# Performance work log

Hardware: AMD Instinct MI355X
Metric: run time of the kernel (lower is better)

Reference implementation:

```python
import jax, jax.numpy as jnp
import numpy as np

B, L, S, H, E = 4, 2048, 2048, 8, 64


def setup_inputs() -> dict:
    key = jax.random.key(0)
    kq, kk, kv, kt = jax.random.split(key, 4)
    queries = jax.random.normal(kq, (B, L, H, E), dtype=jnp.float32)
    keys = jax.random.normal(kk, (B, S, H, E), dtype=jnp.float32)
    values = jax.random.normal(kv, (B, S, H, E), dtype=jnp.float32)
    # de-stationarization log-scale factor, kept small so exp(tau) ~ O(1)
    tau = 0.1 * jax.random.normal(kt, (B, 1, 1, 1), dtype=jnp.float32)
    # causal mask: True above the diagonal (positions to be masked)
    attn_mask = jnp.triu(jnp.ones((L, S), dtype=bool), k=1)
    return {"queries": queries, "keys": keys, "values": values,
            "attn_mask": attn_mask, "tau": tau}


def reference(queries, keys, values, attn_mask, tau):
    # queries: [B,L,H,E], keys/values: [B,S,H,E], tau: [B,1,1,1], mask: [L,S]
    E_ = queries.shape[-1]
    scale = 1.0 / jnp.sqrt(jnp.asarray(E_, dtype=queries.dtype))
    # scores: [B,H,L,S], with tau-based de-stationarization rescale
    scores = jnp.einsum('blhe,bshe->bhls', queries, keys) * (scale * jnp.exp(tau))
    scores = jnp.where(attn_mask, -jnp.inf, scores)
    A = jax.nn.softmax(scores, axis=-1)  # dropout is identity at inference
    V = jnp.einsum('bhls,bshd->blhd', A, values)
    return V
```

## Files before the change

### kernel.cpp

```cpp
#include <hip/hip_runtime.h>
#include <hip/hip_bf16.h>
#include <math.h>

#define B_ 4
#define L_ 2048
#define H_ 8
#define E_ 64
#define HE 512

typedef short bf16x8 __attribute__((ext_vector_type(8)));
typedef float f32x4 __attribute__((ext_vector_type(4)));
typedef float f32x2 __attribute__((ext_vector_type(2)));
typedef unsigned short u16x4 __attribute__((ext_vector_type(4)));
typedef unsigned short u16x8 __attribute__((ext_vector_type(8)));

__device__ __forceinline__ unsigned short f2b(float f) {
  return __builtin_bit_cast(unsigned short, (__hip_bfloat16)f);
}

__global__ __launch_bounds__(512, 4) void attn_fwd(
    const float* __restrict__ Q, const float* __restrict__ K,
    const float* __restrict__ V, const float* __restrict__ tau,
    float* __restrict__ O)
{
  const int f  = blockIdx.x + 16 * (blockIdx.y + 8 * blockIdx.z);
  const int u  = f >> 5, hb = f & 31;
  const int h  = hb & 7, b = hb >> 3;
  const int qt = (u < 8) ? u : 23 - u;

  const int tid  = threadIdx.x;
  const int wave = tid >> 6, lane = tid & 63;
  const int lg = lane >> 4, ll = lane & 15;
  const int llm = ll & 7;

  __shared__ unsigned short ldsK[2][64 * 64];
  __shared__ unsigned short ldsV[2][64 * 64];

  const float qscale = 0.125f * expf(tau[b]) * 1.44269504088896f;
  const int q0w = qt * 128 + wave * 16;

  const float* Qb = Q + (((size_t)b * L_ + (q0w + ll)) * H_ + h) * E_;
  bf16x8 qf[2];
  #pragma unroll
  for (int ek = 0; ek < 2; ++ek) {
    f32x4 a = *(const f32x4*)(Qb + ek * 32 + lg * 8);
    f32x4 c = *(const f32x4*)(Qb + ek * 32 + lg * 8 + 4);
    #pragma unroll
    for (int j = 0; j < 4; ++j) {
      qf[ek][j]     = (short)f2b(a[j] * qscale);
      qf[ek][4 + j] = (short)f2b(c[j] * qscale);
    }
  }

  float m_run = -INFINITY, l_run = 0.0f;
  f32x4 oacc[4];
  #pragma unroll
  for (int n = 0; n < 4; ++n) {
    oacc[n][0] = 0.f; oacc[n][1] = 0.f; oacc[n][2] = 0.f; oacc[n][3] = 0.f;
  }

  const int krow = tid >> 3;
  const int vq = tid >> 5,  vc = (tid & 31) * 2;
  const float* Kp = K + ((size_t)b * L_ * H_ + h) * E_ + (size_t)krow * HE + (tid & 7) * 8;
  const float* Vp = V + ((size_t)b * L_ * H_ + h) * E_ + (size_t)(4 * vq) * HE + vc;
  const int kw_off = krow * 64 + (((tid & 7) ^ (krow & 7)) << 3);

  const int nt = 2 * qt + 2;
  const int tmaxw = 2 * qt + (wave >> 2);

  {
    f32x4 k0 = *(const f32x4*)(Kp);
    f32x4 k1 = *(const f32x4*)(Kp + 4);
    f32x2 v0 = *(const f32x2*)(Vp);
    f32x2 v1 = *(const f32x2*)(Vp + HE);
    f32x2 v2 = *(const f32x2*)(Vp + 2 * HE);
    f32x2 v3 = *(const f32x2*)(Vp + 3 * HE);
    u16x8 kw;
    #pragma unroll
    for (int j = 0; j < 4; ++j) { kw[j] = f2b(k0[j]); kw[4 + j] = f2b(k1[j]); }
    *(u16x8*)(&ldsK[0][kw_off]) = kw;
    #pragma unroll
    for (int jj = 0; jj < 2; ++jj) {
      const int row = vc + jj;
      u16x4 vw;
      vw[0] = f2b(v0[jj]); vw[1] = f2b(v1[jj]);
      vw[2] = f2b(v2[jj]); vw[3] = f2b(v3[jj]);
      *(u16x4*)(&ldsV[0][row * 64 + (((vq >> 1) ^ (row & 7)) << 3) + 4 * (vq & 1)]) = vw;
    }
  }
  __syncthreads();
  int cur = 0;

  for (int t = 0; t < nt; ++t) {
    const bool havenext = (t + 1 < nt);
    f32x4 k0, k1; f32x2 v0, v1, v2, v3;
    if (havenext) {
      const float* Kn = Kp + (size_t)(t + 1) * 64 * HE;
      const float* Vn = Vp + (size_t)(t + 1) * 64 * HE;
      k0 = *(const f32x4*)(Kn);
      k1 = *(const f32x4*)(Kn + 4);
      v0 = *(const f32x2*)(Vn);
      v1 = *(const f32x2*)(Vn + HE);
      v2 = *(const f32x2*)(Vn + 2 * HE);
      v3 = *(const f32x2*)(Vn + 3 * HE);
    }

    if (t <= tmaxw) {
      const unsigned short* Kl = ldsK[cur];
      const unsigned short* Vl = ldsV[cur];

      f32x4 sacc[4];
      #pragma unroll
      for (int m = 0; m < 4; ++m) {
        sacc[m][0] = 0.f; sacc[m][1] = 0.f; sacc[m][2] = 0.f; sacc[m][3] = 0.f;
      }
      __builtin_amdgcn_s_setprio(1);
      #pragma unroll
      for (int ek = 0; ek < 2; ++ek) {
        #pragma unroll
        for (int m = 0; m < 4; ++m) {
          bf16x8 kf = *(const bf16x8*)(Kl + (16 * m + ll) * 64 +
                                       ((((ek << 2) + lg) ^ llm) << 3));
          sacc[m] = __builtin_amdgcn_mfma_f32_16x16x32_bf16(kf, qf[ek], sacc[m], 0, 0, 0);
        }
      }
      __builtin_amdgcn_s_setprio(0);

      if (t == tmaxw) {
        const int dq = q0w + ll - 64 * t;
        #pragma unroll
        for (int m = 0; m < 4; ++m)
          #pragma unroll
          for (int r = 0; r < 4; ++r)
            if (16 * m + 4 * lg + r > dq) sacc[m][r] = -3.0e38f;
      }

      float t0 = fmaxf(fmaxf(sacc[0][0], sacc[0][1]), fmaxf(sacc[0][2], sacc[0][3]));
      float t1 = fmaxf(fmaxf(sacc[1][0], sacc[1][1]), fmaxf(sacc[1][2], sacc[1][3]));
      float t2 = fmaxf(fmaxf(sacc[2][0], sacc[2][1]), fmaxf(sacc[2][2], sacc[2][3]));
      float t3 = fmaxf(fmaxf(sacc[3][0], sacc[3][1]), fmaxf(sacc[3][2], sacc[3][3]));
      float mx = fmaxf(fmaxf(t0, t1), fmaxf(t2, t3));
      mx = fmaxf(mx, __shfl_xor(mx, 16));
      mx = fmaxf(mx, __shfl_xor(mx, 32));

      if (!__all(mx - m_run <= 8.0f)) {
        const float mnew = fmaxf(m_run, mx);
        const float corr = exp2f(m_run - mnew);
        m_run = mnew;
        l_run *= corr;
        #pragma unroll
        for (int r = 0; r < 4; ++r) {
          const float cr = __shfl(corr, 4 * lg + r);
          #pragma unroll
          for (int n = 0; n < 4; ++n) oacc[n][r] *= cr;
        }
      }

      #pragma unroll
      for (int m = 0; m < 4; ++m)
        #pragma unroll
        for (int r = 0; r < 4; ++r)
          sacc[m][r] = exp2f(sacc[m][r] - m_run);

      float s0 = (sacc[0][0] + sacc[0][1]) + (sacc[0][2] + sacc[0][3]);
      float s1 = (sacc[1][0] + sacc[1][1]) + (sacc[1][2] + sacc[1][3]);
      float s2 = (sacc[2][0] + sacc[2][1]) + (sacc[2][2] + sacc[2][3]);
      float s3 = (sacc[3][0] + sacc[3][1]) + (sacc[3][2] + sacc[3][3]);
      float rs = (s0 + s1) + (s2 + s3);
      rs += __shfl_xor(rs, 16);
      rs += __shfl_xor(rs, 32);
      l_run += rs;

      bf16x8 pf[2];
      #pragma unroll
      for (int ek = 0; ek < 2; ++ek)
        #pragma unroll
        for (int r = 0; r < 4; ++r) {
          pf[ek][r]     = (short)f2b(sacc[2 * ek][r]);
          pf[ek][4 + r] = (short)f2b(sacc[2 * ek + 1][r]);
        }

      __builtin_amdgcn_s_setprio(1);
      #pragma unroll
      for (int ek = 0; ek < 2; ++ek) {
        #pragma unroll
        for (int n = 0; n < 4; ++n) {
          const int d = 16 * n + ll;
          const int base = d * 64 + 4 * (lg & 1);
          union { bf16x8 v8; u16x4 q[2]; } vu;
          vu.q[0] = *(const u16x4*)(Vl + base +
                       ((((ek << 2) + (lg >> 1)) ^ llm) << 3));
          vu.q[1] = *(const u16x4*)(Vl + base +
                       ((((ek << 2) + 2 + (lg >> 1)) ^ llm) << 3));
          oacc[n] = __builtin_amdgcn_mfma_f32_16x16x32_bf16(pf[ek], vu.v8, oacc[n], 0, 0, 0);
        }
      }
      __builtin_amdgcn_s_setprio(0);
    }

    if (havenext) {
      const int nb = cur ^ 1;
      u16x8 kw;
      #pragma unroll
      for (int j = 0; j < 4; ++j) { kw[j] = f2b(k0[j]); kw[4 + j] = f2b(k1[j]); }
      *(u16x8*)(&ldsK[nb][kw_off]) = kw;
      #pragma unroll
      for (int jj = 0; jj < 2; ++jj) {
        const int row = vc + jj;
        u16x4 vw;
        vw[0] = f2b(v0[jj]); vw[1] = f2b(v1[jj]);
        vw[2] = f2b(v2[jj]); vw[3] = f2b(v3[jj]);
        *(u16x4*)(&ldsV[nb][row * 64 + (((vq >> 1) ^ (row & 7)) << 3) + 4 * (vq & 1)]) = vw;
      }
      __syncthreads();
      cur = nb;
    }
  }

  const float linv = 1.0f / l_run;
  float* Ob = O + (((size_t)b * L_ + q0w) * H_ + h) * E_;
  #pragma unroll
  for (int r = 0; r < 4; ++r) {
    const float inv = __shfl(linv, 4 * lg + r);
    const int qrow = 4 * lg + r;
    #pragma unroll
    for (int n = 0; n < 4; ++n)
      Ob[(size_t)qrow * HE + 16 * n + ll] = oacc[n][r] * inv;
  }
}

extern "C" void kernel_launch(void* const* d_in, const int* in_sizes, int n_in,
                              void* d_out, int out_size, void* d_ws, size_t ws_size,
                              hipStream_t stream) {
  (void)in_sizes; (void)n_in; (void)out_size; (void)d_ws; (void)ws_size;
  const float* Q   = (const float*)d_in[0];
  const float* K   = (const float*)d_in[1];
  const float* V   = (const float*)d_in[2];
  const float* tau = (const float*)d_in[4];
  float* O = (float*)d_out;
  dim3 grid(L_ / 128, H_, B_), block(512);
  hipLaunchKernelGGL(attn_fwd, grid, block, 0, stream, Q, K, V, tau, O);
}
```

Measured before the change: 60.26 us.

## Switch attention to 32x32x16 MFMA with 4 waves of 32 query rows

Replaces the 16x16x32 bf16 MFMA tiling with 32x32x16 MFMA, so each wave handles 32 query rows and the block shrinks from 8 to 4 waves. P is converted to bf16 with packed v_cvt_pk_bf16_f32 and rearranged through v_permlane32_swap so it can feed the PV MFMA from registers. K/V staging loads are widened to full float4 per thread. Larger MFMA tiles cut LDS fragment reads and cross-lane reductions per FLOP, but each wave holds more accumulator registers and there are fewer waves per block to hide latency.

```diff
diff --git a/kernel.cpp b/kernel.cpp
--- a/kernel.cpp
+++ b/kernel.cpp
@@ -10,15 +10,23 @@
 
 typedef short bf16x8 __attribute__((ext_vector_type(8)));
 typedef float f32x4 __attribute__((ext_vector_type(4)));
-typedef float f32x2 __attribute__((ext_vector_type(2)));
+typedef float f32x16 __attribute__((ext_vector_type(16)));
 typedef unsigned short u16x4 __attribute__((ext_vector_type(4)));
 typedef unsigned short u16x8 __attribute__((ext_vector_type(8)));
 
 __device__ __forceinline__ unsigned short f2b(float f) {
   return __builtin_bit_cast(unsigned short, (__hip_bfloat16)f);
 }
-
-__global__ __launch_bounds__(512, 4) void attn_fwd(
+__device__ __forceinline__ unsigned cvtpk(float lo, float hi) {
+  unsigned r;
+  asm("v_cvt_pk_bf16_f32 %0, %1, %2" : "=v"(r) : "v"(lo), "v"(hi));
+  return r;
+}
+__device__ __forceinline__ void pl32swap(unsigned &a, unsigned &b) {
+  asm volatile("v_permlane32_swap_b32 %0, %1" : "+v"(a), "+v"(b));
+}
+
+__global__ __launch_bounds__(256, 2) void attn_fwd(
     const float* __restrict__ Q, const float* __restrict__ K,
     const float* __restrict__ V, const float* __restrict__ tau,
     float* __restrict__ O)
@@ -30,62 +38,67 @@
 
   const int tid  = threadIdx.x;
   const int wave = tid >> 6, lane = tid & 63;
-  const int lg = lane >> 4, ll = lane & 15;
-  const int llm = ll & 7;
+  const int l31 = lane & 31, hi = lane >> 5;
+  const int l7 = l31 & 7;
 
   __shared__ unsigned short ldsK[2][64 * 64];
   __shared__ unsigned short ldsV[2][64 * 64];
 
   const float qscale = 0.125f * expf(tau[b]) * 1.44269504088896f;
-  const int q0w = qt * 128 + wave * 16;
-
-  const float* Qb = Q + (((size_t)b * L_ + (q0w + ll)) * H_ + h) * E_;
-  bf16x8 qf[2];
+  const int q0w = qt * 128 + wave * 32;
+  const int myq = q0w + l31;
+
+  const float* Qb = Q + (((size_t)b * L_ + myq) * H_ + h) * E_;
+  bf16x8 qf[4];
   #pragma unroll
-  for (int ek = 0; ek < 2; ++ek) {
-    f32x4 a = *(const f32x4*)(Qb + ek * 32 + lg * 8);
-    f32x4 c = *(const f32x4*)(Qb + ek * 32 + lg * 8 + 4);
+  for (int ks = 0; ks < 4; ++ks) {
+    f32x4 a = *(const f32x4*)(Qb + ks * 16 + hi * 8);
+    f32x4 c = *(const f32x4*)(Qb + ks * 16 + hi * 8 + 4);
     #pragma unroll
     for (int j = 0; j < 4; ++j) {
-      qf[ek][j]     = (short)f2b(a[j] * qscale);
-      qf[ek][4 + j] = (short)f2b(c[j] * qscale);
+      qf[ks][j]     = (short)f2b(a[j] * qscale);
+      qf[ks][4 + j] = (short)f2b(c[j] * qscale);
     }
   }
 
   float m_run = -INFINITY, l_run = 0.0f;
-  f32x4 oacc[4];
+  f32x16 oacc[2];
   #pragma unroll
-  for (int n = 0; n < 4; ++n) {
-    oacc[n][0] = 0.f; oacc[n][1] = 0.f; oacc[n][2] = 0.f; oacc[n][3] = 0.f;
-  }
-
-  const int krow = tid >> 3;
-  const int vq = tid >> 5,  vc = (tid & 31) * 2;
-  const float* Kp = K + ((size_t)b * L_ * H_ + h) * E_ + (size_t)krow * HE + (tid & 7) * 8;
-  const float* Vp = V + ((size_t)b * L_ * H_ + h) * E_ + (size_t)(4 * vq) * HE + vc;
-  const int kw_off = krow * 64 + (((tid & 7) ^ (krow & 7)) << 3);
+  for (int nd = 0; nd < 2; ++nd)
+    #pragma unroll
+    for (int r = 0; r < 16; ++r) oacc[nd][r] = 0.0f;
+
+  const int krow = tid >> 2, kcg = tid & 3;
+  const int vkv = (tid & 15) * 4, vd = (tid >> 4) * 4;
+  const float* Kp = K + ((size_t)b * L_ * H_ + h) * E_ + (size_t)krow * HE + kcg * 16;
+  const float* Vp = V + ((size_t)b * L_ * H_ + h) * E_ + (size_t)vkv * HE + vd;
+  const int kwo0 = krow * 64 + (((2 * kcg) ^ (krow & 7)) << 3);
+  const int kwo1 = krow * 64 + (((2 * kcg + 1) ^ (krow & 7)) << 3);
 
   const int nt = 2 * qt + 2;
-  const int tmaxw = 2 * qt + (wave >> 2);
+  const int tmaxw = 2 * qt + (wave >> 1);
 
   {
-    f32x4 k0 = *(const f32x4*)(Kp);
-    f32x4 k1 = *(const f32x4*)(Kp + 4);
-    f32x2 v0 = *(const f32x2*)(Vp);
-    f32x2 v1 = *(const f32x2*)(Vp + HE);
-    f32x2 v2 = *(const f32x2*)(Vp + 2 * HE);
-    f32x2 v3 = *(const f32x2*)(Vp + 3 * HE);
-    u16x8 kw;
-    #pragma unroll
-    for (int j = 0; j < 4; ++j) { kw[j] = f2b(k0[j]); kw[4 + j] = f2b(k1[j]); }
-    *(u16x8*)(&ldsK[0][kw_off]) = kw;
-    #pragma unroll
-    for (int jj = 0; jj < 2; ++jj) {
-      const int row = vc + jj;
+    f32x4 kq[4], vq[4];
+    #pragma unroll
+    for (int i = 0; i < 4; ++i) kq[i] = *(const f32x4*)(Kp + 4 * i);
+    #pragma unroll
+    for (int i = 0; i < 4; ++i) vq[i] = *(const f32x4*)(Vp + (size_t)i * HE);
+    u16x8 w0, w1;
+    #pragma unroll
+    for (int j = 0; j < 4; ++j) {
+      w0[j] = f2b(kq[0][j]); w0[4 + j] = f2b(kq[1][j]);
+      w1[j] = f2b(kq[2][j]); w1[4 + j] = f2b(kq[3][j]);
+    }
+    *(u16x8*)(&ldsK[0][kwo0]) = w0;
+    *(u16x8*)(&ldsK[0][kwo1]) = w1;
+    #pragma unroll
+    for (int jd = 0; jd < 4; ++jd) {
+      const int row = vd + jd;
       u16x4 vw;
-      vw[0] = f2b(v0[jj]); vw[1] = f2b(v1[jj]);
-      vw[2] = f2b(v2[jj]); vw[3] = f2b(v3[jj]);
-      *(u16x4*)(&ldsV[0][row * 64 + (((vq >> 1) ^ (row & 7)) << 3) + 4 * (vq & 1)]) = vw;
+      #pragma unroll
+      for (int i = 0; i < 4; ++i) vw[i] = f2b(vq[i][jd]);
+      *(u16x4*)(&ldsV[0][row * 64 + (((vkv >> 3) ^ (row & 7)) << 3) + (vkv & 7)]) = vw;
     }
   }
   __syncthreads();
@@ -93,54 +106,60 @@
 
   for (int t = 0; t < nt; ++t) {
     const bool havenext = (t + 1 < nt);
-    f32x4 k0, k1; f32x2 v0, v1, v2, v3;
+    f32x4 kq[4], vq[4];
     if (havenext) {
       const float* Kn = Kp + (size_t)(t + 1) * 64 * HE;
       const float* Vn = Vp + (size_t)(t + 1) * 64 * HE;
-      k0 = *(const f32x4*)(Kn);
-      k1 = *(const f32x4*)(Kn + 4);
-      v0 = *(const f32x2*)(Vn);
-      v1 = *(const f32x2*)(Vn + HE);
-      v2 = *(const f32x2*)(Vn + 2 * HE);
-      v3 = *(const f32x2*)(Vn + 3 * HE);
+      #pragma unroll
+      for (int i = 0; i < 4; ++i) kq[i] = *(const f32x4*)(Kn + 4 * i);
+      #pragma unroll
+      for (int i = 0; i < 4; ++i) vq[i] = *(const f32x4*)(Vn + (size_t)i * HE);
     }
 
     if (t <= tmaxw) {
       const unsigned short* Kl = ldsK[cur];
       const unsigned short* Vl = ldsV[cur];
 
-      f32x4 sacc[4];
-      #pragma unroll
-      for (int m = 0; m < 4; ++m) {
-        sacc[m][0] = 0.f; sacc[m][1] = 0.f; sacc[m][2] = 0.f; sacc[m][3] = 0.f;
-      }
+      f32x16 sacc[2];
+      #pragma unroll
+      for (int mt = 0; mt < 2; ++mt)
+        #pragma unroll
+        for (int r = 0; r < 16; ++r) sacc[mt][r] = 0.0f;
       __builtin_amdgcn_s_setprio(1);
       #pragma unroll
-      for (int ek = 0; ek < 2; ++ek) {
-        #pragma unroll
-        for (int m = 0; m < 4; ++m) {
-          bf16x8 kf = *(const bf16x8*)(Kl + (16 * m + ll) * 64 +
-                                       ((((ek << 2) + lg) ^ llm) << 3));
-          sacc[m] = __builtin_amdgcn_mfma_f32_16x16x32_bf16(kf, qf[ek], sacc[m], 0, 0, 0);
+      for (int ks = 0; ks < 4; ++ks) {
+        #pragma unroll
+        for (int mt = 0; mt < 2; ++mt) {
+          bf16x8 kf = *(const bf16x8*)(Kl + (32 * mt + l31) * 64 +
+                                       (((2 * ks + hi) ^ l7) << 3));
+          sacc[mt] = __builtin_amdgcn_mfma_f32_32x32x16_bf16(kf, qf[ks], sacc[mt], 0, 0, 0);
         }
       }
       __builtin_amdgcn_s_setprio(0);
 
       if (t == tmaxw) {
-        const int dq = q0w + ll - 64 * t;
-        #pragma unroll
-        for (int m = 0; m < 4; ++m)
+        const int dq = myq - 64 * t;
+        const int kvhi = 4 * hi;
+        #pragma unroll
+        for (int mt = 0; mt < 2; ++mt)
           #pragma unroll
-          for (int r = 0; r < 4; ++r)
-            if (16 * m + 4 * lg + r > dq) sacc[m][r] = -3.0e38f;
-      }
-
-      float t0 = fmaxf(fmaxf(sacc[0][0], sacc[0][1]), fmaxf(sacc[0][2], sacc[0][3]));
-      float t1 = fmaxf(fmaxf(sacc[1][0], sacc[1][1]), fmaxf(sacc[1][2], sacc[1][3]));
-      float t2 = fmaxf(fmaxf(sacc[2][0], sacc[2][1]), fmaxf(sacc[2][2], sacc[2][3]));
-      float t3 = fmaxf(fmaxf(sacc[3][0], sacc[3][1]), fmaxf(sacc[3][2], sacc[3][3]));
-      float mx = fmaxf(fmaxf(t0, t1), fmaxf(t2, t3));
-      mx = fmaxf(mx, __shfl_xor(mx, 16));
+          for (int r = 0; r < 16; ++r) {
+            const int kvl = (r & 3) + 8 * (r >> 2) + 32 * mt;
+            if (kvl + kvhi > dq) sacc[mt][r] = -3.0e38f;
+          }
+      }
+
+      float p0 = sacc[0][0], p1 = sacc[0][1], p2 = sacc[0][2], p3 = sacc[0][3];
+      #pragma unroll
+      for (int mt = 0; mt < 2; ++mt)
+        #pragma unroll
+        for (int r = (mt == 0 ? 4 : 0); r < 16; r += 4) {
+          p0 = fmaxf(p0, sacc[mt][r]);
+          p1 = fmaxf(p1, sacc[mt][r + 1]);
+          p2 = fmaxf(p2, sacc[mt][r + 2]);
+          p3 = fmaxf(p3, sacc[mt][r + 3]);
+        }
+      float mx = fmaxf(fmaxf(p0, p1), fmaxf(p2, p3));
       mx = fmaxf(mx, __shfl_xor(mx, 32));
 
       if (!__all(mx - m_run <= 8.0f)) {
@@ -149,50 +168,58 @@
         m_run = mnew;
         l_run *= corr;
         #pragma unroll
-        for (int r = 0; r < 4; ++r) {
-          const float cr = __shfl(corr, 4 * lg + r);
-          #pragma unroll
-          for (int n = 0; n < 4; ++n) oacc[n][r] *= cr;
-        }
-      }
-
-      #pragma unroll
-      for (int m = 0; m < 4; ++m)
-        #pragma unroll
-        for (int r = 0; r < 4; ++r)
-          sacc[m][r] = exp2f(sacc[m][r] - m_run);
-
-      float s0 = (sacc[0][0] + sacc[0][1]) + (sacc[0][2] + sacc[0][3]);
-      float s1 = (sacc[1][0] + sacc[1][1]) + (sacc[1][2] + sacc[1][3]);
-      float s2 = (sacc[2][0] + sacc[2][1]) + (sacc[2][2] + sacc[2][3]);
-      float s3 = (sacc[3][0] + sacc[3][1]) + (sacc[3][2] + sacc[3][3]);
+        for (int r = 0; r < 16; ++r) {
+          const int qrow = (r & 3) + 8 * (r >> 2) + 4 * hi;
+          const float cr = __shfl(corr, qrow);
+          oacc[0][r] *= cr;
+          oacc[1][r] *= cr;
+        }
+      }
+
+      float s0 = 0.f, s1 = 0.f, s2 = 0.f, s3 = 0.f;
+      #pragma unroll
+      for (int mt = 0; mt < 2; ++mt)
+        #pragma unroll
+        for (int r = 0; r < 16; r += 4) {
+          float e0 = exp2f(sacc[mt][r]     - m_run);
+          float e1 = exp2f(sacc[mt][r + 1] - m_run);
+          float e2 = exp2f(sacc[mt][r + 2] - m_run);
+          float e3 = exp2f(sacc[mt][r + 3] - m_run);
+          sacc[mt][r] = e0; sacc[mt][r + 1] = e1;
+          sacc[mt][r + 2] = e2; sacc[mt][r + 3] = e3;
+          s0 += e0; s1 += e1; s2 += e2; s3 += e3;
+        }
       float rs = (s0 + s1) + (s2 + s3);
-      rs += __shfl_xor(rs, 16);
       rs += __shfl_xor(rs, 32);
       l_run += rs;
 
-      bf16x8 pf[2];
-      #pragma unroll
-      for (int ek = 0; ek < 2; ++ek)
-        #pragma unroll
-        for (int r = 0; r < 4; ++r) {
-          pf[ek][r]     = (short)f2b(sacc[2 * ek][r]);
-          pf[ek][4 + r] = (short)f2b(sacc[2 * ek + 1][r]);
-        }
+      unsigned pk0[8], pk1[8];
+      #pragma unroll
+      for (int i = 0; i < 8; ++i) pk0[i] = cvtpk(sacc[0][2 * i], sacc[0][2 * i + 1]);
+      #pragma unroll
+      for (int i = 0; i < 8; ++i) pk1[i] = cvtpk(sacc[1][2 * i], sacc[1][2 * i + 1]);
+      bf16x8 pf[4];
+      #pragma unroll
+      for (int ks = 0; ks < 4; ++ks) {
+        unsigned a  = (ks >> 1) ? pk1[4 * (ks & 1)]     : pk0[4 * (ks & 1)];
+        unsigned y  = (ks >> 1) ? pk1[4 * (ks & 1) + 2] : pk0[4 * (ks & 1) + 2];
+        unsigned a2 = (ks >> 1) ? pk1[4 * (ks & 1) + 1] : pk0[4 * (ks & 1) + 1];
+        unsigned y2 = (ks >> 1) ? pk1[4 * (ks & 1) + 3] : pk0[4 * (ks & 1) + 3];
+        pl32swap(a, y);
+        pl32swap(a2, y2);
+        union { unsigned w[4]; bf16x8 v; } pu;
+        pu.w[0] = a; pu.w[1] = a2; pu.w[2] = y; pu.w[3] = y2;
+        pf[ks] = pu.v;
+      }
 
       __builtin_amdgcn_s_setprio(1);
       #pragma unroll
-      for (int ek = 0; ek < 2; ++ek) {
-        #pragma unroll
-        for (int n = 0; n < 4; ++n) {
-          const int d = 16 * n + ll;
-          const int base = d * 64 + 4 * (lg & 1);
-          union { bf16x8 v8; u16x4 q[2]; } vu;
-          vu.q[0] = *(const u16x4*)(Vl + base +
-                       ((((ek << 2) + (lg >> 1)) ^ llm) << 3));
-          vu.q[1] = *(const u16x4*)(Vl + base +
-                       ((((ek << 2) + 2 + (lg >> 1)) ^ llm) << 3));
-          oacc[n] = __builtin_amdgcn_mfma_f32_16x16x32_bf16(pf[ek], vu.v8, oacc[n], 0, 0, 0);
+      for (int ks = 0; ks < 4; ++ks) {
+        #pragma unroll
+        for (int nd = 0; nd < 2; ++nd) {
+          bf16x8 vf = *(const bf16x8*)(Vl + (32 * nd + l31) * 64 +
+                                       (((2 * ks + hi) ^ l7) << 3));
+          oacc[nd] = __builtin_amdgcn_mfma_f32_32x32x16_bf16(pf[ks], vf, oacc[nd], 0, 0, 0);
         }
       }
       __builtin_amdgcn_s_setprio(0);
@@ -200,17 +227,21 @@
 
     if (havenext) {
       const int nb = cur ^ 1;
-      u16x8 kw;
-      #pragma unroll
-      for (int j = 0; j < 4; ++j) { kw[j] = f2b(k0[j]); kw[4 + j] = f2b(k1[j]); }
-      *(u16x8*)(&ldsK[nb][kw_off]) = kw;
-      #pragma unroll
-      for (int jj = 0; jj < 2; ++jj) {
-        const int row = vc + jj;
+      u16x8 w0, w1;
+      #pragma unroll
+      for (int j = 0; j < 4; ++j) {
+        w0[j] = f2b(kq[0][j]); w0[4 + j] = f2b(kq[1][j]);
+        w1[j] = f2b(kq[2][j]); w1[4 + j] = f2b(kq[3][j]);
+      }
+      *(u16x8*)(&ldsK[nb][kwo0]) = w0;
+      *(u16x8*)(&ldsK[nb][kwo1]) = w1;
+      #pragma unroll
+      for (int jd = 0; jd < 4; ++jd) {
+        const int row = vd + jd;
         u16x4 vw;
-        vw[0] = f2b(v0[jj]); vw[1] = f2b(v1[jj]);
-        vw[2] = f2b(v2[jj]); vw[3] = f2b(v3[jj]);
-        *(u16x4*)(&ldsV[nb][row * 64 + (((vq >> 1) ^ (row & 7)) << 3) + 4 * (vq & 1)]) = vw;
+        #pragma unroll
+        for (int i = 0; i < 4; ++i) vw[i] = f2b(vq[i][jd]);
+        *(u16x4*)(&ldsV[nb][row * 64 + (((vkv >> 3) ^ (row & 7)) << 3) + (vkv & 7)]) = vw;
       }
       __syncthreads();
       cur = nb;
@@ -220,12 +251,11 @@
   const float linv = 1.0f / l_run;
   float* Ob = O + (((size_t)b * L_ + q0w) * H_ + h) * E_;
   #pragma unroll
-  for (int r = 0; r < 4; ++r) {
-    const float inv = __shfl(linv, 4 * lg + r);
-    const int qrow = 4 * lg + r;
-    #pragma unroll
-    for (int n = 0; n < 4; ++n)
-      Ob[(size_t)qrow * HE + 16 * n + ll] = oacc[n][r] * inv;
+  for (int r = 0; r < 16; ++r) {
+    const int qrow = (r & 3) + 8 * (r >> 2) + 4 * hi;
+    const float inv = __shfl(linv, qrow);
+    Ob[(size_t)qrow * HE + l31]      = oacc[0][r] * inv;
+    Ob[(size_t)qrow * HE + 32 + l31] = oacc[1][r] * inv;
   }
 }
 
@@ -238,6 +268,6 @@
   const float* V   = (const float*)d_in[2];
   const float* tau = (const float*)d_in[4];
   float* O = (float*)d_out;
-  dim3 grid(L_ / 128, H_, B_), block(512);
+  dim3 grid(L_ / 128, H_, B_), block(256);
   hipLaunchKernelGGL(attn_fwd, grid, block, 0, stream, Q, K, V, tau, O);
 }
```

Measured after the change: 60.08 us. About the same (-0.3%).

## Split causal KV range into two balanced phases per block with combine kernel

Applied to the files above, without the earlier changes.

Each block now handles two query tiles, the short tile j and part of the long tile 15-j, so every block does about the same number of KV tiles. The long tile's remaining KV range is finished by another block, and its partial output plus running max and sum are written to workspace. A second kernel then merges the two partial softmax states per row. This targets the causal load imbalance in the old grid, at the cost of an extra launch, extra global traffic for partials, and a change of launch bounds to 1.

```diff
diff --git a/kernel.cpp b/kernel.cpp
--- a/kernel.cpp
+++ b/kernel.cpp
@@ -18,15 +18,16 @@
   return __builtin_bit_cast(unsigned short, (__hip_bfloat16)f);
 }
 
-__global__ __launch_bounds__(512, 4) void attn_fwd(
+__global__ __launch_bounds__(512, 1) void attn_fwd(
     const float* __restrict__ Q, const float* __restrict__ K,
     const float* __restrict__ V, const float* __restrict__ tau,
-    float* __restrict__ O)
+    float* __restrict__ O, float* __restrict__ wsOB,
+    float* __restrict__ mA, float* __restrict__ lA,
+    float* __restrict__ mB, float* __restrict__ lB)
 {
   const int f  = blockIdx.x + 16 * (blockIdx.y + 8 * blockIdx.z);
-  const int u  = f >> 5, hb = f & 31;
+  const int j  = f >> 5, hb = f & 31;
   const int h  = hb & 7, b = hb >> 3;
-  const int qt = (u < 8) ? u : 23 - u;
 
   const int tid  = threadIdx.x;
   const int wave = tid >> 6, lane = tid & 63;
@@ -37,207 +38,232 @@
   __shared__ unsigned short ldsV[2][64 * 64];
 
   const float qscale = 0.125f * expf(tau[b]) * 1.44269504088896f;
-  const int q0w = qt * 128 + wave * 16;
-
-  const float* Qb = Q + (((size_t)b * L_ + (q0w + ll)) * H_ + h) * E_;
-  bf16x8 qf[2];
-  #pragma unroll
-  for (int ek = 0; ek < 2; ++ek) {
-    f32x4 a = *(const f32x4*)(Qb + ek * 32 + lg * 8);
-    f32x4 c = *(const f32x4*)(Qb + ek * 32 + lg * 8 + 4);
+
+  const int krow = tid >> 3, kc8 = tid & 7;
+  const int vrow = tid >> 5, vc = (tid & 31) * 2;
+  const size_t bh = ((size_t)b * L_ * H_ + h) * E_;
+  const int kw_off = krow * 64 + ((kc8 ^ (krow & 7)) << 3);
+
+  auto run_phase = [&](int jj, int t0, int t1,
+                       float* Opart, float* mout, float* lout) {
+    const int q0w = jj * 128 + wave * 16;
+    const int tmaxw = 2 * jj + (wave >> 2);
+
+    const float* Qb = Q + (((size_t)b * L_ + (q0w + ll)) * H_ + h) * E_;
+    bf16x8 qf[2];
     #pragma unroll
-    for (int j = 0; j < 4; ++j) {
-      qf[ek][j]     = (short)f2b(a[j] * qscale);
-      qf[ek][4 + j] = (short)f2b(c[j] * qscale);
-    }
-  }
-
-  float m_run = -INFINITY, l_run = 0.0f;
-  f32x4 oacc[4];
-  #pragma unroll
-  for (int n = 0; n < 4; ++n) {
-    oacc[n][0] = 0.f; oacc[n][1] = 0.f; oacc[n][2] = 0.f; oacc[n][3] = 0.f;
-  }
-
-  const int krow = tid >> 3;
-  const int vq = tid >> 5,  vc = (tid & 31) * 2;
-  const float* Kp = K + ((size_t)b * L_ * H_ + h) * E_ + (size_t)krow * HE + (tid & 7) * 8;
-  const float* Vp = V + ((size_t)b * L_ * H_ + h) * E_ + (size_t)(4 * vq) * HE + vc;
-  const int kw_off = krow * 64 + (((tid & 7) ^ (krow & 7)) << 3);
-
-  const int nt = 2 * qt + 2;
-  const int tmaxw = 2 * qt + (wave >> 2);
-
-  {
-    f32x4 k0 = *(const f32x4*)(Kp);
-    f32x4 k1 = *(const f32x4*)(Kp + 4);
-    f32x2 v0 = *(const f32x2*)(Vp);
-    f32x2 v1 = *(const f32x2*)(Vp + HE);
-    f32x2 v2 = *(const f32x2*)(Vp + 2 * HE);
-    f32x2 v3 = *(const f32x2*)(Vp + 3 * HE);
-    u16x8 kw;
+    for (int ek = 0; ek < 2; ++ek) {
+      f32x4 a = *(const f32x4*)(Qb + ek * 32 + lg * 8);
+      f32x4 c = *(const f32x4*)(Qb + ek * 32 + lg * 8 + 4);
+      #pragma unroll
+      for (int jd = 0; jd < 4; ++jd) {
+        qf[ek][jd]     = (short)f2b(a[jd] * qscale);
+        qf[ek][4 + jd] = (short)f2b(c[jd] * qscale);
+      }
+    }
+
+    float m_run = -INFINITY, l_run = 0.0f;
+    f32x4 oacc[4];
     #pragma unroll
-    for (int j = 0; j < 4; ++j) { kw[j] = f2b(k0[j]); kw[4 + j] = f2b(k1[j]); }
-    *(u16x8*)(&ldsK[0][kw_off]) = kw;
-    #pragma unroll
-    for (int jj = 0; jj < 2; ++jj) {
-      const int row = vc + jj;
-      u16x4 vw;
-      vw[0] = f2b(v0[jj]); vw[1] = f2b(v1[jj]);
-      vw[2] = f2b(v2[jj]); vw[3] = f2b(v3[jj]);
-      *(u16x4*)(&ldsV[0][row * 64 + (((vq >> 1) ^ (row & 7)) << 3) + 4 * (vq & 1)]) = vw;
-    }
-  }
-  __syncthreads();
-  int cur = 0;
-
-  for (int t = 0; t < nt; ++t) {
-    const bool havenext = (t + 1 < nt);
+    for (int n = 0; n < 4; ++n) {
+      oacc[n][0] = 0.f; oacc[n][1] = 0.f; oacc[n][2] = 0.f; oacc[n][3] = 0.f;
+    }
+
     f32x4 k0, k1; f32x2 v0, v1, v2, v3;
-    if (havenext) {
-      const float* Kn = Kp + (size_t)(t + 1) * 64 * HE;
-      const float* Vn = Vp + (size_t)(t + 1) * 64 * HE;
+    auto load_tile = [&](int t) {
+      const float* Kn = K + bh + (size_t)(64 * t + krow) * HE + kc8 * 8;
+      const float* Vn = V + bh + (size_t)(64 * t + 4 * vrow) * HE + vc;
       k0 = *(const f32x4*)(Kn);
       k1 = *(const f32x4*)(Kn + 4);
       v0 = *(const f32x2*)(Vn);
       v1 = *(const f32x2*)(Vn + HE);
       v2 = *(const f32x2*)(Vn + 2 * HE);
       v3 = *(const f32x2*)(Vn + 3 * HE);
-    }
-
-    if (t <= tmaxw) {
-      const unsigned short* Kl = ldsK[cur];
-      const unsigned short* Vl = ldsV[cur];
-
-      f32x4 sacc[4];
-      #pragma unroll
-      for (int m = 0; m < 4; ++m) {
-        sacc[m][0] = 0.f; sacc[m][1] = 0.f; sacc[m][2] = 0.f; sacc[m][3] = 0.f;
-      }
-      __builtin_amdgcn_s_setprio(1);
-      #pragma unroll
-      for (int ek = 0; ek < 2; ++ek) {
-        #pragma unroll
-        for (int m = 0; m < 4; ++m) {
-          bf16x8 kf = *(const bf16x8*)(Kl + (16 * m + ll) * 64 +
-                                       ((((ek << 2) + lg) ^ llm) << 3));
-          sacc[m] = __builtin_amdgcn_mfma_f32_16x16x32_bf16(kf, qf[ek], sacc[m], 0, 0, 0);
-        }
-      }
-      __builtin_amdgcn_s_setprio(0);
-
-      if (t == tmaxw) {
-        const int dq = q0w + ll - 64 * t;
+    };
+    auto stage_write = [&](int nb) {
+      u16x8 kw;
+      #pragma unroll
+      for (int jd = 0; jd < 4; ++jd) { kw[jd] = f2b(k0[jd]); kw[4 + jd] = f2b(k1[jd]); }
+      *(u16x8*)(&ldsK[nb][kw_off]) = kw;
+      #pragma unroll
+      for (int jj2 = 0; jj2 < 2; ++jj2) {
+        const int row = vc + jj2;
+        u16x4 vw;
+        vw[0] = f2b(v0[jj2]); vw[1] = f2b(v1[jj2]);
+        vw[2] = f2b(v2[jj2]); vw[3] = f2b(v3[jj2]);
+        *(u16x4*)(&ldsV[nb][row * 64 + (((vrow >> 1) ^ (row & 7)) << 3) + 4 * (vrow & 1)]) = vw;
+      }
+    };
+
+    __syncthreads();
+    load_tile(t0);
+    stage_write(0);
+    __syncthreads();
+    int cur = 0;
+
+    for (int t = t0; t < t1; ++t) {
+      const bool havenext = (t + 1 < t1);
+      if (havenext) load_tile(t + 1);
+
+      if (t <= tmaxw) {
+        const unsigned short* Kl = ldsK[cur];
+        const unsigned short* Vl = ldsV[cur];
+
+        f32x4 sacc[4];
+        #pragma unroll
+        for (int n = 0; n < 4; ++n) {
+          sacc[n][0] = 0.f; sacc[n][1] = 0.f; sacc[n][2] = 0.f; sacc[n][3] = 0.f;
+        }
+        __builtin_amdgcn_s_setprio(1);
+        #pragma unroll
+        for (int ek = 0; ek < 2; ++ek) {
+          #pragma unroll
+          for (int n = 0; n < 4; ++n) {
+            bf16x8 kf = *(const bf16x8*)(Kl + (16 * n + ll) * 64 +
+                                         ((((ek << 2) + lg) ^ llm) << 3));
+            sacc[n] = __builtin_amdgcn_mfma_f32_16x16x32_bf16(kf, qf[ek], sacc[n], 0, 0, 0);
+          }
+        }
+        __builtin_amdgcn_s_setprio(0);
+
+        if (t == tmaxw) {
+          const int dq = q0w + ll - 64 * t;
+          #pragma unroll
+          for (int m = 0; m < 4; ++m)
+            #pragma unroll
+            for (int r = 0; r < 4; ++r)
+              if (16 * m + 4 * lg + r > dq) sacc[m][r] = -3.0e38f;
+        }
+
+        float t0m = fmaxf(fmaxf(sacc[0][0], sacc[0][1]), fmaxf(sacc[0][2], sacc[0][3]));
+        float t1m = fmaxf(fmaxf(sacc[1][0], sacc[1][1]), fmaxf(sacc[1][2], sacc[1][3]));
+        float t2m = fmaxf(fmaxf(sacc[2][0], sacc[2][1]), fmaxf(sacc[2][2], sacc[2][3]));
+        float t3m = fmaxf(fmaxf(sacc[3][0], sacc[3][1]), fmaxf(sacc[3][2], sacc[3][3]));
+        float mx = fmaxf(fmaxf(t0m, t1m), fmaxf(t2m, t3m));
+        mx = fmaxf(mx, __shfl_xor(mx, 16));
+        mx = fmaxf(mx, __shfl_xor(mx, 32));
+
+        if (!__all(mx - m_run <= 8.0f)) {
+          const float mnew = fmaxf(m_run, mx);
+          const float corr = exp2f(m_run - mnew);
+          m_run = mnew;
+          l_run *= corr;
+          #pragma unroll
+          for (int r = 0; r < 4; ++r) {
+            const float cr = __shfl(corr, 4 * lg + r);
+            #pragma unroll
+            for (int n = 0; n < 4; ++n) oacc[n][r] *= cr;
+          }
+        }
+
         #pragma unroll
         for (int m = 0; m < 4; ++m)
           #pragma unroll
           for (int r = 0; r < 4; ++r)
-            if (16 * m + 4 * lg + r > dq) sacc[m][r] = -3.0e38f;
-      }
-
-      float t0 = fmaxf(fmaxf(sacc[0][0], sacc[0][1]), fmaxf(sacc[0][2], sacc[0][3]));
-      float t1 = fmaxf(fmaxf(sacc[1][0], sacc[1][1]), fmaxf(sacc[1][2], sacc[1][3]));
-      float t2 = fmaxf(fmaxf(sacc[2][0], sacc[2][1]), fmaxf(sacc[2][2], sacc[2][3]));
-      float t3 = fmaxf(fmaxf(sacc[3][0], sacc[3][1]), fmaxf(sacc[3][2], sacc[3][3]));
-      float mx = fmaxf(fmaxf(t0, t1), fmaxf(t2, t3));
-      mx = fmaxf(mx, __shfl_xor(mx, 16));
-      mx = fmaxf(mx, __shfl_xor(mx, 32));
-
-      if (!__all(mx - m_run <= 8.0f)) {
-        const float mnew = fmaxf(m_run, mx);
-        const float corr = exp2f(m_run - mnew);
-        m_run = mnew;
-        l_run *= corr;
-        #pragma unroll
-        for (int r = 0; r < 4; ++r) {
-          const float cr = __shfl(corr, 4 * lg + r);
-          #pragma unroll
-          for (int n = 0; n < 4; ++n) oacc[n][r] *= cr;
-        }
-      }
-
-      #pragma unroll
-      for (int m = 0; m < 4; ++m)
-        #pragma unroll
-        for (int r = 0; r < 4; ++r)
-          sacc[m][r] = exp2f(sacc[m][r] - m_run);
-
-      float s0 = (sacc[0][0] + sacc[0][1]) + (sacc[0][2] + sacc[0][3]);
-      float s1 = (sacc[1][0] + sacc[1][1]) + (sacc[1][2] + sacc[1][3]);
-      float s2 = (sacc[2][0] + sacc[2][1]) + (sacc[2][2] + sacc[2][3]);
-      float s3 = (sacc[3][0] + sacc[3][1]) + (sacc[3][2] + sacc[3][3]);
-      float rs = (s0 + s1) + (s2 + s3);
-      rs += __shfl_xor(rs, 16);
-      rs += __shfl_xor(rs, 32);
-      l_run += rs;
-
-      bf16x8 pf[2];
-      #pragma unroll
-      for (int ek = 0; ek < 2; ++ek)
-        #pragma unroll
-        for (int r = 0; r < 4; ++r) {
-          pf[ek][r]     = (short)f2b(sacc[2 * ek][r]);
-          pf[ek][4 + r] = (short)f2b(sacc[2 * ek + 1][r]);
-        }
-
-      __builtin_amdgcn_s_setprio(1);
-      #pragma unroll
-      for (int ek = 0; ek < 2; ++ek) {
-        #pragma unroll
-        for (int n = 0; n < 4; ++n) {
-          const int d = 16 * n + ll;
-          const int base = d * 64 + 4 * (lg & 1);
-          union { bf16x8 v8; u16x4 q[2]; } vu;
-          vu.q[0] = *(const u16x4*)(Vl + base +
-                       ((((ek << 2) + (lg >> 1)) ^ llm) << 3));
-          vu.q[1] = *(const u16x4*)(Vl + base +
-                       ((((ek << 2) + 2 + (lg >> 1)) ^ llm) << 3));
-          oacc[n] = __builtin_amdgcn_mfma_f32_16x16x32_bf16(pf[ek], vu.v8, oacc[n], 0, 0, 0);
-        }
-      }
-      __builtin_amdgcn_s_setprio(0);
-    }
-
-    if (havenext) {
-      const int nb = cur ^ 1;
-      u16x8 kw;
-      #pragma unroll
-      for (int j = 0; j < 4; ++j) { kw[j] = f2b(k0[j]); kw[4 + j] = f2b(k1[j]); }
-      *(u16x8*)(&ldsK[nb][kw_off]) = kw;
-      #pragma unroll
-      for (int jj = 0; jj < 2; ++jj) {
-        const int row = vc + jj;
-        u16x4 vw;
-        vw[0] = f2b(v0[jj]); vw[1] = f2b(v1[jj]);
-        vw[2] = f2b(v2[jj]); vw[3] = f2b(v3[jj]);
-        *(u16x4*)(&ldsV[nb][row * 64 + (((vq >> 1) ^ (row & 7)) << 3) + 4 * (vq & 1)]) = vw;
-      }
-      __syncthreads();
-      cur = nb;
-    }
-  }
-
-  const float linv = 1.0f / l_run;
-  float* Ob = O + (((size_t)b * L_ + q0w) * H_ + h) * E_;
+            sacc[m][r] = exp2f(sacc[m][r] - m_run);
+
+        float s0 = (sacc[0][0] + sacc[0][1]) + (sacc[0][2] + sacc[0][3]);
+        float s1 = (sacc[1][0] + sacc[1][1]) + (sacc[1][2] + sacc[1][3]);
+        float s2 = (sacc[2][0] + sacc[2][1]) + (sacc[2][2] + sacc[2][3]);
+        float s3 = (sacc[3][0] + sacc[3][1]) + (sacc[3][2] + sacc[3][3]);
+        float rs = (s0 + s1) + (s2 + s3);
+        rs += __shfl_xor(rs, 16);
+        rs += __shfl_xor(rs, 32);
+        l_run += rs;
+
+        bf16x8 pf[2];
+        #pragma unroll
+        for (int ek = 0; ek < 2; ++ek)
+          #pragma unroll
+          for (int r = 0; r < 4; ++r) {
+            pf[ek][r]     = (short)f2b(sacc[2 * ek][r]);
+            pf[ek][4 + r] = (short)f2b(sacc[2 * ek + 1][r]);
+          }
+
+        __builtin_amdgcn_s_setprio(1);
+        #pragma unroll
+        for (int ek = 0; ek < 2; ++ek) {
+          #pragma unroll
+          for (int n = 0; n < 4; ++n) {
+            const int d = 16 * n + ll;
+            const int base = d * 64 + 4 * (lg & 1);
+            union { bf16x8 v8; u16x4 q[2]; } vu;
+            vu.q[0] = *(const u16x4*)(Vl + base +
+                         ((((ek << 2) + (lg >> 1)) ^ llm) << 3));
+            vu.q[1] = *(const u16x4*)(Vl + base +
+                         ((((ek << 2) + 2 + (lg >> 1)) ^ llm) << 3));
+            oacc[n] = __builtin_amdgcn_mfma_f32_16x16x32_bf16(pf[ek], vu.v8, oacc[n], 0, 0, 0);
+          }
+        }
+        __builtin_amdgcn_s_setprio(0);
+      }
+
+      if (havenext) {
+        stage_write(cur ^ 1);
+        __syncthreads();
+        cur ^= 1;
+      }
+    }
+
+    float* Ob = Opart + (((size_t)b * L_ + q0w) * H_ + h) * E_;
+    #pragma unroll
+    for (int r = 0; r < 4; ++r) {
+      const int qrow = lg * 4 + r;
+      #pragma unroll
+      for (int n = 0; n < 4; ++n)
+        Ob[(size_t)qrow * HE + n * 16 + ll] = oacc[n][r];
+    }
+    if (lg == 0) {
+      const int qh = (b * L_ + q0w + ll) * H_ + h;
+      mout[qh] = m_run;
+      lout[qh] = l_run;
+    }
+  };
+
+  run_phase(j, 0, j + 1, O, mA, lA);
+  run_phase(15 - j, 16 - j, 32 - 2 * j, wsOB, mB, lB);
+}
+
+__global__ __launch_bounds__(256) void attn_combine(
+    float* __restrict__ O, const float* __restrict__ wsOB,
+    const float* __restrict__ mA, const float* __restrict__ lA,
+    const float* __restrict__ mB, const float* __restrict__ lB)
+{
+  const int idx = blockIdx.x * 256 + threadIdx.x;
+  const int qh = idx >> 4;
+  const float ma = mA[qh], la = lA[qh];
+  const float mb = mB[qh], lb = lB[qh];
+  const float m = fmaxf(ma, mb);
+  const float wa = exp2f(ma - m), wb = exp2f(mb - m);
+  const float inv = 1.0f / (wa * la + wb * lb);
+  const f32x4 oa = ((const f32x4*)O)[idx];
+  const f32x4 ob = ((const f32x4*)wsOB)[idx];
+  f32x4 out;
   #pragma unroll
-  for (int r = 0; r < 4; ++r) {
-    const float inv = __shfl(linv, 4 * lg + r);
-    const int qrow = 4 * lg + r;
-    #pragma unroll
-    for (int n = 0; n < 4; ++n)
-      Ob[(size_t)qrow * HE + 16 * n + ll] = oacc[n][r] * inv;
-  }
+  for (int i = 0; i < 4; ++i) out[i] = (oa[i] * wa + ob[i] * wb) * inv;
+  ((f32x4*)O)[idx] = out;
 }
 
 extern "C" void kernel_launch(void* const* d_in, const int* in_sizes, int n_in,
                               void* d_out, int out_size, void* d_ws, size_t ws_size,
                               hipStream_t stream) {
-  (void)in_sizes; (void)n_in; (void)out_size; (void)d_ws; (void)ws_size;
+  (void)in_sizes; (void)n_in; (void)out_size; (void)ws_size;
   const float* Q   = (const float*)d_in[0];
   const float* K   = (const float*)d_in[1];
   const float* V   = (const float*)d_in[2];
   const float* tau = (const float*)d_in[4];
   float* O = (float*)d_out;
-  dim3 grid(L_ / 128, H_, B_), block(512);
-  hipLaunchKernelGGL(attn_fwd, grid, block, 0, stream, Q, K, V, tau, O);
-}
+
+  float* wsOB = (float*)d_ws;
+  float* mA = wsOB + (size_t)B_ * L_ * H_ * E_;
+  float* lA = mA + (size_t)B_ * L_ * H_;
+  float* mB = lA + (size_t)B_ * L_ * H_;
+  float* lB = mB + (size_t)B_ * L_ * H_;
+
+  dim3 grid(16, 8, 4), block(512);
+  hipLaunchKernelGGL(attn_fwd, grid, block, 0, stream,
+                     Q, K, V, tau, O, wsOB, mA, lA, mB, lB);
+  const int total4 = B_ * L_ * H_ * E_ / 4;
+  hipLaunchKernelGGL(attn_combine, dim3(total4 / 256), dim3(256), 0, stream,
+                     O, wsOB, mA, lA, mB, lB);
+}
```

After: 60.31 us. About the same (+0.1%).

## Split KV sequence across two wave halves with 64-row query tiles and LDS combine

Applied to the files above, without the earlier changes.

Each block now handles 64 query rows instead of 128. The two halves of the block's waves process alternating 32-key tiles and merge their partial softmax states through shared memory at the end. This doubles the grid to 1024 blocks, uses a new causal-balanced tile order and raises launch bounds occupancy to 6. It also switches P packing to v_cvt_pk_bf16_f32 and uses a padded V layout. The aim is better load balance and occupancy, at the cost of an extra LDS combine pass and smaller MFMA tiles per wave.

```diff
diff --git a/kernel.cpp b/kernel.cpp
--- a/kernel.cpp
+++ b/kernel.cpp
@@ -17,27 +17,36 @@
 __device__ __forceinline__ unsigned short f2b(float f) {
   return __builtin_bit_cast(unsigned short, (__hip_bfloat16)f);
 }
-
-__global__ __launch_bounds__(512, 4) void attn_fwd(
+__device__ __forceinline__ unsigned cvtpk(float lo, float hi) {
+  unsigned r;
+  asm("v_cvt_pk_bf16_f32 %0, %1, %2" : "=v"(r) : "v"(lo), "v"(hi));
+  return r;
+}
+
+__global__ __launch_bounds__(512, 6) void attn_fwd(
     const float* __restrict__ Q, const float* __restrict__ K,
     const float* __restrict__ V, const float* __restrict__ tau,
     float* __restrict__ O)
 {
-  const int f  = blockIdx.x + 16 * (blockIdx.y + 8 * blockIdx.z);
-  const int u  = f >> 5, hb = f & 31;
+  const int hb = blockIdx.x;
   const int h  = hb & 7, b = hb >> 3;
-  const int qt = (u < 8) ? u : 23 - u;
+  const int u  = blockIdx.y + 8 * blockIdx.z;
+  const int qt = (u < 8) ? u : (u < 16) ? 39 - u : (u < 24) ? u - 8 : 47 - u;
 
   const int tid  = threadIdx.x;
   const int wave = tid >> 6, lane = tid & 63;
-  const int lg = lane >> 4, ll = lane & 15;
-  const int llm = ll & 7;
-
-  __shared__ unsigned short ldsK[2][64 * 64];
-  __shared__ unsigned short ldsV[2][64 * 64];
+  const int lg = lane >> 4, ll = lane & 15, llm = ll & 7;
+  const int half = wave >> 2, wv = wave & 3;
+
+  __shared__ union {
+    struct { unsigned short Kt[2][2][32 * 64];
+             unsigned short Vt[2][2][64 * 36]; } kv;
+    struct { float O[64][64]; float m[64]; float l[64]; } cmb;
+  } sm;
 
   const float qscale = 0.125f * expf(tau[b]) * 1.44269504088896f;
-  const int q0w = qt * 128 + wave * 16;
+  const int q0w = qt * 64 + wv * 16;
+  const int tmaxw = 2 * qt + (wv >> 1);
 
   const float* Qb = Q + (((size_t)b * L_ + (q0w + ll)) * H_ + h) * E_;
   bf16x8 qf[2];
@@ -46,9 +55,9 @@
     f32x4 a = *(const f32x4*)(Qb + ek * 32 + lg * 8);
     f32x4 c = *(const f32x4*)(Qb + ek * 32 + lg * 8 + 4);
     #pragma unroll
-    for (int j = 0; j < 4; ++j) {
-      qf[ek][j]     = (short)f2b(a[j] * qscale);
-      qf[ek][4 + j] = (short)f2b(c[j] * qscale);
+    for (int jd = 0; jd < 4; ++jd) {
+      qf[ek][jd]     = (short)f2b(a[jd] * qscale);
+      qf[ek][4 + jd] = (short)f2b(c[jd] * qscale);
     }
   }
 
@@ -59,66 +68,63 @@
     oacc[n][0] = 0.f; oacc[n][1] = 0.f; oacc[n][2] = 0.f; oacc[n][3] = 0.f;
   }
 
-  const int krow = tid >> 3;
-  const int vq = tid >> 5,  vc = (tid & 31) * 2;
-  const float* Kp = K + ((size_t)b * L_ * H_ + h) * E_ + (size_t)krow * HE + (tid & 7) * 8;
-  const float* Vp = V + ((size_t)b * L_ * H_ + h) * E_ + (size_t)(4 * vq) * HE + vc;
-  const int kw_off = krow * 64 + (((tid & 7) ^ (krow & 7)) << 3);
-
-  const int nt = 2 * qt + 2;
-  const int tmaxw = 2 * qt + (wave >> 2);
-
-  {
-    f32x4 k0 = *(const f32x4*)(Kp);
-    f32x4 k1 = *(const f32x4*)(Kp + 4);
-    f32x2 v0 = *(const f32x2*)(Vp);
-    f32x2 v1 = *(const f32x2*)(Vp + HE);
-    f32x2 v2 = *(const f32x2*)(Vp + 2 * HE);
-    f32x2 v3 = *(const f32x2*)(Vp + 3 * HE);
+  const int hs = tid >> 8, st = tid & 255;
+  const int krow = st >> 3, kc8 = st & 7;
+  const int vrow = st >> 5, vc = (st & 31) * 2;
+  const size_t bh = ((size_t)b * L_ * H_ + h) * E_;
+  const int kw_off = krow * 64 + ((kc8 ^ (krow & 7)) << 3);
+
+  f32x4 k0, k1; f32x2 v0, v1, v2, v3;
+  auto load_tile = [&](int t32) {
+    const float* Kn = K + bh + (size_t)(32 * t32 + krow) * HE + kc8 * 8;
+    const float* Vn = V + bh + (size_t)(32 * t32 + 4 * vrow) * HE + vc;
+    k0 = *(const f32x4*)(Kn);
+    k1 = *(const f32x4*)(Kn + 4);
+    v0 = *(const f32x2*)(Vn);
+    v1 = *(const f32x2*)(Vn + HE);
+    v2 = *(const f32x2*)(Vn + 2 * HE);
+    v3 = *(const f32x2*)(Vn + 3 * HE);
+  };
+  auto stage_write = [&](int nb) {
     u16x8 kw;
     #pragma unroll
-    for (int j = 0; j < 4; ++j) { kw[j] = f2b(k0[j]); kw[4 + j] = f2b(k1[j]); }
-    *(u16x8*)(&ldsK[0][kw_off]) = kw;
+    for (int jd = 0; jd < 4; ++jd) { kw[jd] = f2b(k0[jd]); kw[4 + jd] = f2b(k1[jd]); }
+    *(u16x8*)(&sm.kv.Kt[hs][nb][kw_off]) = kw;
     #pragma unroll
     for (int jj = 0; jj < 2; ++jj) {
       const int row = vc + jj;
       u16x4 vw;
       vw[0] = f2b(v0[jj]); vw[1] = f2b(v1[jj]);
       vw[2] = f2b(v2[jj]); vw[3] = f2b(v3[jj]);
-      *(u16x4*)(&ldsV[0][row * 64 + (((vq >> 1) ^ (row & 7)) << 3) + 4 * (vq & 1)]) = vw;
-    }
-  }
+      *(u16x4*)(&sm.kv.Vt[hs][nb][row * 36 + 4 * vrow]) = vw;
+    }
+  };
+
+  const int niter = qt + 1;
+  load_tile(hs);
+  stage_write(0);
   __syncthreads();
   int cur = 0;
 
-  for (int t = 0; t < nt; ++t) {
-    const bool havenext = (t + 1 < nt);
-    f32x4 k0, k1; f32x2 v0, v1, v2, v3;
-    if (havenext) {
-      const float* Kn = Kp + (size_t)(t + 1) * 64 * HE;
-      const float* Vn = Vp + (size_t)(t + 1) * 64 * HE;
-      k0 = *(const f32x4*)(Kn);
-      k1 = *(const f32x4*)(Kn + 4);
-      v0 = *(const f32x2*)(Vn);
-      v1 = *(const f32x2*)(Vn + HE);
-      v2 = *(const f32x2*)(Vn + 2 * HE);
-      v3 = *(const f32x2*)(Vn + 3 * HE);
-    }
+  for (int i = 0; i < niter; ++i) {
+    const int t = 2 * i + half;
+    const bool havenext = (i + 1 < niter);
+    if (havenext) load_tile(2 * (i + 1) + hs);
 
     if (t <= tmaxw) {
-      const unsigned short* Kl = ldsK[cur];
-      const unsigned short* Vl = ldsV[cur];
-
-      f32x4 sacc[4];
-      #pragma unroll
-      for (int m = 0; m < 4; ++m) {
+      const unsigned short* Kl = sm.kv.Kt[half][cur];
+      const unsigned short* Vl = sm.kv.Vt[half][cur];
+
+      f32x4 sacc[2];
+      #pragma unroll
+      for (int m = 0; m < 2; ++m) {
         sacc[m][0] = 0.f; sacc[m][1] = 0.f; sacc[m][2] = 0.f; sacc[m][3] = 0.f;
       }
       __builtin_amdgcn_s_setprio(1);
       #pragma unroll
       for (int ek = 0; ek < 2; ++ek) {
         #pragma unroll
-        for (int m = 0; m < 4; ++m) {
+        for (int m = 0; m < 2; ++m) {
           bf16x8 kf = *(const bf16x8*)(Kl + (16 * m + ll) * 64 +
                                        ((((ek << 2) + lg) ^ llm) << 3));
           sacc[m] = __builtin_amdgcn_mfma_f32_16x16x32_bf16(kf, qf[ek], sacc[m], 0, 0, 0);
@@ -127,19 +133,17 @@
       __builtin_amdgcn_s_setprio(0);
 
       if (t == tmaxw) {
-        const int dq = q0w + ll - 64 * t;
-        #pragma unroll
-        for (int m = 0; m < 4; ++m)
+        const int dq = q0w + ll - 32 * t;
+        #pragma unroll
+        for (int m = 0; m < 2; ++m)
           #pragma unroll
           for (int r = 0; r < 4; ++r)
             if (16 * m + 4 * lg + r > dq) sacc[m][r] = -3.0e38f;
       }
 
-      float t0 = fmaxf(fmaxf(sacc[0][0], sacc[0][1]), fmaxf(sacc[0][2], sacc[0][3]));
-      float t1 = fmaxf(fmaxf(sacc[1][0], sacc[1][1]), fmaxf(sacc[1][2], sacc[1][3]));
-      float t2 = fmaxf(fmaxf(sacc[2][0], sacc[2][1]), fmaxf(sacc[2][2], sacc[2][3]));
-      float t3 = fmaxf(fmaxf(sacc[3][0], sacc[3][1]), fmaxf(sacc[3][2], sacc[3][3]));
-      float mx = fmaxf(fmaxf(t0, t1), fmaxf(t2, t3));
+      float m0 = fmaxf(fmaxf(sacc[0][0], sacc[0][1]), fmaxf(sacc[0][2], sacc[0][3]));
+      float m1 = fmaxf(fmaxf(sacc[1][0], sacc[1][1]), fmaxf(sacc[1][2], sacc[1][3]));
+      float mx = fmaxf(m0, m1);
       mx = fmaxf(mx, __shfl_xor(mx, 16));
       mx = fmaxf(mx, __shfl_xor(mx, 32));
 
@@ -157,75 +161,73 @@
       }
 
       #pragma unroll
-      for (int m = 0; m < 4; ++m)
+      for (int m = 0; m < 2; ++m)
         #pragma unroll
         for (int r = 0; r < 4; ++r)
           sacc[m][r] = exp2f(sacc[m][r] - m_run);
 
-      float s0 = (sacc[0][0] + sacc[0][1]) + (sacc[0][2] + sacc[0][3]);
-      float s1 = (sacc[1][0] + sacc[1][1]) + (sacc[1][2] + sacc[1][3]);
-      float s2 = (sacc[2][0] + sacc[2][1]) + (sacc[2][2] + sacc[2][3]);
-      float s3 = (sacc[3][0] + sacc[3][1]) + (sacc[3][2] + sacc[3][3]);
-      float rs = (s0 + s1) + (s2 + s3);
+      float rs = ((sacc[0][0] + sacc[0][1]) + (sacc[0][2] + sacc[0][3]))
+               + ((sacc[1][0] + sacc[1][1]) + (sacc[1][2] + sacc[1][3]));
       rs += __shfl_xor(rs, 16);
       rs += __shfl_xor(rs, 32);
       l_run += rs;
 
-      bf16x8 pf[2];
-      #pragma unroll
-      for (int ek = 0; ek < 2; ++ek)
-        #pragma unroll
-        for (int r = 0; r < 4; ++r) {
-          pf[ek][r]     = (short)f2b(sacc[2 * ek][r]);
-          pf[ek][4 + r] = (short)f2b(sacc[2 * ek + 1][r]);
-        }
+      union { unsigned w[4]; bf16x8 v; } pu;
+      pu.w[0] = cvtpk(sacc[0][0], sacc[0][1]);
+      pu.w[1] = cvtpk(sacc[0][2], sacc[0][3]);
+      pu.w[2] = cvtpk(sacc[1][0], sacc[1][1]);
+      pu.w[3] = cvtpk(sacc[1][2], sacc[1][3]);
 
       __builtin_amdgcn_s_setprio(1);
       #pragma unroll
-      for (int ek = 0; ek < 2; ++ek) {
-        #pragma unroll
-        for (int n = 0; n < 4; ++n) {
-          const int d = 16 * n + ll;
-          const int base = d * 64 + 4 * (lg & 1);
-          union { bf16x8 v8; u16x4 q[2]; } vu;
-          vu.q[0] = *(const u16x4*)(Vl + base +
-                       ((((ek << 2) + (lg >> 1)) ^ llm) << 3));
-          vu.q[1] = *(const u16x4*)(Vl + base +
-                       ((((ek << 2) + 2 + (lg >> 1)) ^ llm) << 3));
-          oacc[n] = __builtin_amdgcn_mfma_f32_16x16x32_bf16(pf[ek], vu.v8, oacc[n], 0, 0, 0);
-        }
+      for (int n = 0; n < 4; ++n) {
+        const int d = 16 * n + ll;
+        union { bf16x8 v8; u16x4 q[2]; } vu;
+        vu.q[0] = *(const u16x4*)(Vl + d * 36 + 4 * lg);
+        vu.q[1] = *(const u16x4*)(Vl + d * 36 + 16 + 4 * lg);
+        oacc[n] = __builtin_amdgcn_mfma_f32_16x16x32_bf16(pu.v, vu.v8, oacc[n], 0, 0, 0);
       }
       __builtin_amdgcn_s_setprio(0);
     }
 
     if (havenext) {
-      const int nb = cur ^ 1;
-      u16x8 kw;
-      #pragma unroll
-      for (int j = 0; j < 4; ++j) { kw[j] = f2b(k0[j]); kw[4 + j] = f2b(k1[j]); }
-      *(u16x8*)(&ldsK[nb][kw_off]) = kw;
-      #pragma unroll
-      for (int jj = 0; jj < 2; ++jj) {
-        const int row = vc + jj;
-        u16x4 vw;
-        vw[0] = f2b(v0[jj]); vw[1] = f2b(v1[jj]);
-        vw[2] = f2b(v2[jj]); vw[3] = f2b(v3[jj]);
-        *(u16x4*)(&ldsV[nb][row * 64 + (((vq >> 1) ^ (row & 7)) << 3) + 4 * (vq & 1)]) = vw;
-      }
+      stage_write(cur ^ 1);
       __syncthreads();
-      cur = nb;
-    }
-  }
-
-  const float linv = 1.0f / l_run;
-  float* Ob = O + (((size_t)b * L_ + q0w) * H_ + h) * E_;
-  #pragma unroll
-  for (int r = 0; r < 4; ++r) {
-    const float inv = __shfl(linv, 4 * lg + r);
-    const int qrow = 4 * lg + r;
-    #pragma unroll
-    for (int n = 0; n < 4; ++n)
-      Ob[(size_t)qrow * HE + 16 * n + ll] = oacc[n][r] * inv;
+      cur ^= 1;
+    }
+  }
+
+  __syncthreads();
+  if (half == 1) {
+    #pragma unroll
+    for (int r = 0; r < 4; ++r) {
+      const int qrow = 4 * lg + r;
+      #pragma unroll
+      for (int n = 0; n < 4; ++n)
+        sm.cmb.O[16 * wv + qrow][16 * n + ll] = oacc[n][r];
+    }
+    if (lg == 0) { sm.cmb.m[16 * wv + ll] = m_run; sm.cmb.l[16 * wv + ll] = l_run; }
+  }
+  __syncthreads();
+  if (half == 0) {
+    const float m_b = sm.cmb.m[16 * wv + ll];
+    const float l_b = sm.cmb.l[16 * wv + ll];
+    const float mm = fmaxf(m_run, m_b);
+    const float sa = exp2f(m_run - mm);
+    const float sb = exp2f(m_b - mm);
+    const float linv = 1.0f / (sa * l_run + sb * l_b);
+    const float wa = sa * linv, wb = sb * linv;
+    float* Ob = O + (((size_t)b * L_ + q0w) * H_ + h) * E_;
+    #pragma unroll
+    for (int r = 0; r < 4; ++r) {
+      const int qrow = 4 * lg + r;
+      const float wa_r = __shfl(wa, qrow);
+      const float wb_r = __shfl(wb, qrow);
+      #pragma unroll
+      for (int n = 0; n < 4; ++n)
+        Ob[(size_t)qrow * HE + 16 * n + ll] =
+            wa_r * oacc[n][r] + wb_r * sm.cmb.O[16 * wv + qrow][16 * n + ll];
+    }
   }
 }
 
@@ -238,6 +240,6 @@
   const float* V   = (const float*)d_in[2];
   const float* tau = (const float*)d_in[4];
   float* O = (float*)d_out;
-  dim3 grid(L_ / 128, H_, B_), block(512);
+  dim3 grid(32, 8, 4), block(512);
   hipLaunchKernelGGL(attn_fwd, grid, block, 0, stream, Q, K, V, tau, O);
 }
```

After: 58.90 us. 2.2% less time.
